# Kernel tuning notes

Measured on AMD Instinct MI355X. Metric: run time of the kernel, lower is better.

## Reference

```python
import jax, jax.numpy as jnp
import numpy as np

LATENT_DIM = 256
BOOK_SIZE = 8192


def setup_inputs() -> dict:
    key = jax.random.key(0)
    k1, k2 = jax.random.split(key)
    z_e = jax.random.normal(k1, (16, LATENT_DIM, 32, 32), dtype=jnp.float32)
    codebook = jax.random.normal(k2, (BOOK_SIZE, LATENT_DIM), dtype=jnp.float32)
    return {"z_e": z_e, "codebook": codebook}


def reference(z_e, codebook):
    # NCHW -> NHWC -> (B*H*W, D)
    flat_z = jnp.transpose(z_e, (0, 2, 3, 1)).reshape(-1, LATENT_DIM)
    # squared euclidean distance via matmul: ||z||^2 + ||e||^2 - 2 z.e
    dist = (
        jnp.sum(flat_z ** 2, axis=1, keepdims=True)
        + jnp.sum(codebook ** 2, axis=1)
        - 2.0 * flat_z @ codebook.T
    )  # (N, book_size)
    indices = jnp.argmin(dist, axis=1)          # (N,)
    z_q = codebook[indices]                      # (N, D) gather
    return z_q, indices
```

## Files before the change

### kernel.cpp

```cpp
#include <hip/hip_runtime.h>
#include <stdint.h>

#define NROWS 16384
#define NCODES 8192
#define DIM 256
#define EPS_S 0.4f
#define SM 0.8f

typedef __attribute__((ext_vector_type(8))) short bf16x8;
typedef __attribute__((ext_vector_type(4))) float f32x4;
typedef unsigned int uint32;

__device__ __forceinline__ unsigned short f2bf(float f) {
  union { float f; unsigned int u; } v; v.f = f;
  unsigned int u = v.u;
  return (unsigned short)((u + 0x7FFFu + ((u >> 16) & 1u)) >> 16);
}

__device__ __forceinline__ void glds16(const void* g, void* l) {
  __builtin_amdgcn_global_load_lds(
      (const __attribute__((address_space(1))) unsigned int*)g,
      (__attribute__((address_space(3))) unsigned int*)l, 16, 0, 0);
}

__device__ __forceinline__ unsigned long long packdi(float d, int idx) {
  unsigned int u = __float_as_uint(d);
  u = (u & 0x80000000u) ? ~u : (u | 0x80000000u);
  return ((unsigned long long)u << 32) | (unsigned int)idx;
}
__device__ __forceinline__ unsigned long long u64min(unsigned long long a,
                                                     unsigned long long b) {
  return a < b ? a : b;
}
__device__ __forceinline__ unsigned long long shflx64(unsigned long long v, int m) {
  int lo = __shfl_xor((int)(unsigned int)v, m);
  int hi = __shfl_xor((int)(v >> 32), m);
  return ((unsigned long long)(unsigned int)hi << 32) | (unsigned int)lo;
}
__device__ __forceinline__ uint32 umax(uint32 a, uint32 b) { return a > b ? a : b; }
__device__ __forceinline__ uint32 umin(uint32 a, uint32 b) { return a < b ? a : b; }

__global__ __launch_bounds__(256) void prep_z(const float* __restrict__ z,
                                              float* __restrict__ flatz,
                                              ushort* __restrict__ zb) {
  __shared__ float t[32][33];
  const int tx = threadIdx.x & 31, ty = threadIdx.x >> 5;
  const int b = blockIdx.z, ct = blockIdx.y, ht = blockIdx.x;
  const float* src = z + (size_t)b * 262144 + (size_t)(ct * 32) * 1024 + ht * 32;
#pragma unroll
  for (int i = 0; i < 4; ++i) {
    int c = ty + i * 8;
    t[c][tx] = src[c * 1024 + tx];
  }
  __syncthreads();
#pragma unroll
  for (int i = 0; i < 4; ++i) {
    int hw = ty + i * 8;
    int row = b * 1024 + ht * 32 + hw;
    float v = t[tx][hw];
    flatz[(size_t)row * 256 + ct * 32 + tx] = v;
    zb[(size_t)row * 256 + ct * 32 + tx] = f2bf(v);
  }
}

__global__ __launch_bounds__(256) void prep_cb(const float* __restrict__ cb,
                                               ushort* __restrict__ eb,
                                               float* __restrict__ enorm) {
  const int lane = threadIdx.x & 63, wave = threadIdx.x >> 6;
  const int code = blockIdx.x * 4 + wave;
  float4 v = *(const float4*)(cb + (size_t)code * 256 + lane * 4);
  ushort4 o;
  o.x = f2bf(v.x); o.y = f2bf(v.y); o.z = f2bf(v.z); o.w = f2bf(v.w);
  *(ushort4*)(eb + (size_t)code * 256 + lane * 4) = o;
  float ss = v.x * v.x + v.y * v.y + v.z * v.z + v.w * v.w;
#pragma unroll
  for (int s = 1; s < 64; s <<= 1) ss += __shfl_xor(ss, s);
  if (lane == 0) enorm[code] = ss;
}

__global__ __launch_bounds__(256) void vq_gemm(const ushort* __restrict__ eb,
                                               const ushort* __restrict__ zb,
                                               const float* __restrict__ enorm,
                                               uint32* __restrict__ bm) {
  __shared__ __align__(16) ushort As[2][4096];
  __shared__ __align__(16) ushort Bs[2][4096];
  const int tid = threadIdx.x;
  const int wave = tid >> 6, lane = tid & 63;
  const int wr = wave >> 1, wc = wave & 1;
  const int code0 = blockIdx.x * 128;
  const int zrow0 = blockIdx.y * 128;
  const int q = lane >> 4, l15 = lane & 15;
  const int slot = (q ^ ((l15 >> 1) & 3)) * 8;

  f32x4 acc[4][4];
#pragma unroll
  for (int i = 0; i < 4; ++i) {
    float4 e = *(const float4*)(enorm + code0 + wr * 64 + i * 16 + q * 4);
    f32x4 c0 = {1024.f - 0.5f * e.x, 1024.f - 0.5f * e.y,
                1024.f - 0.5f * e.z, 1024.f - 0.5f * e.w};
#pragma unroll
    for (int j = 0; j < 4; ++j) acc[i][j] = c0;
  }

  const int r_in = lane >> 2;
  const int kc = (lane & 3) ^ ((lane >> 3) & 3);
  const ushort* aG0 = eb + (size_t)(code0 + wave * 16 + r_in) * 256 + kc * 8;
  const ushort* aG1 = eb + (size_t)(code0 + 64 + wave * 16 + r_in) * 256 + kc * 8;
  const ushort* bG0 = zb + (size_t)(zrow0 + wave * 16 + r_in) * 256 + kc * 8;
  const ushort* bG1 = zb + (size_t)(zrow0 + 64 + wave * 16 + r_in) * 256 + kc * 8;

  glds16(aG0, &As[0][wave * 512]);
  glds16(aG1, &As[0][(wave + 4) * 512]);
  glds16(bG0, &Bs[0][wave * 512]);
  glds16(bG1, &Bs[0][(wave + 4) * 512]);

#pragma unroll
  for (int k0 = 0; k0 < 8; ++k0) {
    const int cur = k0 & 1;
    __syncthreads();
    if (k0 < 7) {
      glds16(aG0 + (k0 + 1) * 32, &As[cur ^ 1][wave * 512]);
      glds16(aG1 + (k0 + 1) * 32, &As[cur ^ 1][(wave + 4) * 512]);
      glds16(bG0 + (k0 + 1) * 32, &Bs[cur ^ 1][wave * 512]);
      glds16(bG1 + (k0 + 1) * 32, &Bs[cur ^ 1][(wave + 4) * 512]);
    }
    bf16x8 af[4], bf[4];
#pragma unroll
    for (int i = 0; i < 4; ++i)
      af[i] = *(const bf16x8*)(&As[cur][(wr * 64 + i * 16 + l15) * 32 + slot]);
#pragma unroll
    for (int j = 0; j < 4; ++j)
      bf[j] = *(const bf16x8*)(&Bs[cur][(wc * 64 + j * 16 + l15) * 32 + slot]);
#pragma unroll
    for (int i = 0; i < 4; ++i)
#pragma unroll
      for (int j = 0; j < 4; ++j)
        acc[i][j] = __builtin_amdgcn_mfma_f32_16x16x32_bf16(af[i], bf[j],
                                                            acc[i][j], 0, 0, 0);
  }

  const int cid0 = blockIdx.x * 8 + wr * 4;
#pragma unroll
  for (int j = 0; j < 4; ++j) {
    uint32 res[4];
#pragma unroll
    for (int i = 0; i < 4; ++i) {
      uint32 pv0 = (__float_as_uint(acc[i][j][0]) & ~31u) | (uint32)(q * 4 + 0);
      uint32 pv1 = (__float_as_uint(acc[i][j][1]) & ~31u) | (uint32)(q * 4 + 1);
      uint32 pv2 = (__float_as_uint(acc[i][j][2]) & ~31u) | (uint32)(q * 4 + 2);
      uint32 pv3 = (__float_as_uint(acc[i][j][3]) & ~31u) | (uint32)(q * 4 + 3);
      uint32 x01 = umax(pv0, pv1), n01 = umin(pv0, pv1);
      uint32 x23 = umax(pv2, pv3), n23 = umin(pv2, pv3);
      uint32 m1 = umax(x01, x23);
      uint32 m2 = umax(umin(x01, x23), umax(n01, n23));
#pragma unroll
      for (int m = 16; m < 64; m <<= 1) {
        uint32 o1 = (uint32)__shfl_xor((int)m1, m);
        uint32 o2 = (uint32)__shfl_xor((int)m2, m);
        m2 = umax(umax(m2, o2), umin(m1, o1));
        m1 = umax(m1, o1);
      }
      float s1 = __uint_as_float(m1 & ~31u);
      float s2 = __uint_as_float(m2 & ~31u);
      res[i] = (s1 - s2 > SM) ? (m1 | 16u) : m1;
    }
    if (lane < 16) {
      int zr = zrow0 + wc * 64 + j * 16 + l15;
      uint4 o; o.x = res[0]; o.y = res[1]; o.z = res[2]; o.w = res[3];
      *(uint4*)(bm + (size_t)zr * 512 + cid0) = o;
    }
  }
}

__device__ __forceinline__ unsigned long long chunk_exact(
    int chunk, const float* __restrict__ zrow, const float* __restrict__ cb,
    const float* __restrict__ enorm, int lane) {
  const int code = chunk * 16 + (lane >> 2);
  const float* zp = zrow + (lane & 3) * 64;
  const float* cp = cb + (size_t)code * 256 + (lane & 3) * 64;
  float s = 0.f;
#pragma unroll
  for (int d = 0; d < 64; d += 4) {
    float4 zv = *(const float4*)(zp + d);
    float4 cv = *(const float4*)(cp + d);
    s = fmaf(zv.x, cv.x, s); s = fmaf(zv.y, cv.y, s);
    s = fmaf(zv.z, cv.z, s); s = fmaf(zv.w, cv.w, s);
  }
  s += __shfl_xor(s, 1);
  s += __shfl_xor(s, 2);
  float dist = fmaf(-2.f, s, enorm[code]);
  unsigned long long key = ((lane & 3) == 0) ? packdi(dist, code) : ~0ull;
#pragma unroll
  for (int m = 1; m < 64; m <<= 1) key = u64min(key, shflx64(key, m));
  return key;
}

__global__ __launch_bounds__(256) void vq_sel(const uint32* __restrict__ bm,
                                              const float* __restrict__ flatz,
                                              const float* __restrict__ cb,
                                              const float* __restrict__ enorm,
                                              float* __restrict__ zq,
                                              float* __restrict__ oidx) {
  const int lane = threadIdx.x & 63;
  const int row = blockIdx.x * 4 + (threadIdx.x >> 6);
  uint4 va = *(const uint4*)(bm + (size_t)row * 512 + lane * 8);
  uint4 vb = *(const uint4*)(bm + (size_t)row * 512 + lane * 8 + 4);
  uint32 v[8] = {va.x, va.y, va.z, va.w, vb.x, vb.y, vb.z, vb.w};
  uint32 m1 = 0, m2 = 0; int ch = 0;
#pragma unroll
  for (int s = 0; s < 8; ++s) {
    uint32 pv = v[s];
    m2 = umax(m2, umin(m1, pv));
    ch = (pv > m1) ? (lane * 8 + s) : ch;
    m1 = umax(m1, pv);
  }
#pragma unroll
  for (int m = 1; m < 64; m <<= 1) {
    uint32 o1 = (uint32)__shfl_xor((int)m1, m);
    uint32 o2 = (uint32)__shfl_xor((int)m2, m);
    int oc = __shfl_xor(ch, m);
    m2 = umax(umax(m2, o2), umin(m1, o1));
    ch = (o1 > m1) ? oc : ch;
    m1 = umax(m1, o1);
  }
  float s1 = __uint_as_float(m1 & ~31u);
  float s2 = __uint_as_float(m2 & ~31u);
  int idx;
  if ((m1 & 16u) && (s1 - s2 > SM)) {
    idx = ch * 16 + (int)(m1 & 15u);
  } else {
    const float* zrow = flatz + (size_t)row * 256;
    unsigned long long key = chunk_exact(ch, zrow, cb, enorm, lane);
    float dbest;
    { unsigned int u = (unsigned int)(key >> 32);
      u = (u & 0x80000000u) ? (u & 0x7FFFFFFFu) : ~u;
      dbest = __uint_as_float(u); }
    float thr = (1024.f - 0.5f * dbest) - EPS_S;
#pragma unroll
    for (int s = 0; s < 8; ++s) {
      bool cand = __uint_as_float(v[s] & ~31u) >= thr;
      unsigned long long mk = __ballot(cand);
      while (mk) {
        int L = __ffsll(mk) - 1;
        mk &= mk - 1;
        int c2 = L * 8 + s;
        if (c2 == ch) continue;
        key = u64min(key, chunk_exact(c2, zrow, cb, enorm, lane));
      }
    }
    idx = (int)(key & 0xFFFFFFFFull);
  }
  if (lane == 0) oidx[row] = (float)idx;
  float4 val = *(const float4*)(cb + (size_t)idx * 256 + lane * 4);
  *(float4*)(zq + (size_t)row * 256 + lane * 4) = val;
}

extern "C" void kernel_launch(void* const* d_in, const int* in_sizes, int n_in,
                              void* d_out, int out_size, void* d_ws, size_t ws_size,
                              hipStream_t stream) {
  const float* z = (const float*)d_in[0];
  const float* cb = (const float*)d_in[1];
  char* ws = (char*)d_ws;
  ushort* zb = (ushort*)(ws);
  ushort* eb = (ushort*)(ws + (8u << 20));
  float* enorm = (float*)(ws + (12u << 20));
  uint32* bm = (uint32*)(ws + (13u << 20));
  float* zq = (float*)d_out;
  float* oidx = zq + (size_t)NROWS * DIM;
  float* flatz = zq;

  prep_z<<<dim3(32, 8, 16), 256, 0, stream>>>(z, flatz, zb);
  prep_cb<<<NCODES / 4, 256, 0, stream>>>(cb, eb, enorm);
  vq_gemm<<<dim3(NCODES / 128, NROWS / 128), 256, 0, stream>>>(eb, zb, enorm, bm);
  vq_sel<<<NROWS / 4, 256, 0, stream>>>(bm, flatz, cb, enorm, zq, oidx);
}
```

Measured before the change: 207.3 us.

## Switch GEMM to 32x32x16 MFMA tiles and merge prep kernels

Replaces the 16x16x32 bf16 MFMA tiling in vq_gemm with 32x32x16 MFMA instructions, using 2x2 accumulator tiles of 16 floats each. The LDS fragment loads, the swizzle and the per-16-code top-2 selection epilogue are reworked to match the new accumulator layout. The two prep kernels are also fused into one launch, which removes a kernel launch. The larger MFMA means fewer LDS reads and shuffles per FLOP, but the lane-to-code index mapping has to be exactly right for the bitmask output to stay correct.

```diff
diff --git a/kernel.cpp b/kernel.cpp
--- a/kernel.cpp
+++ b/kernel.cpp
@@ -8,7 +8,7 @@
 #define SM 0.8f
 
 typedef __attribute__((ext_vector_type(8))) short bf16x8;
-typedef __attribute__((ext_vector_type(4))) float f32x4;
+typedef __attribute__((ext_vector_type(16))) float f32x16;
 typedef unsigned int uint32;
 
 __device__ __forceinline__ unsigned short f2bf(float f) {
@@ -40,42 +40,44 @@
 __device__ __forceinline__ uint32 umax(uint32 a, uint32 b) { return a > b ? a : b; }
 __device__ __forceinline__ uint32 umin(uint32 a, uint32 b) { return a < b ? a : b; }
 
-__global__ __launch_bounds__(256) void prep_z(const float* __restrict__ z,
-                                              float* __restrict__ flatz,
-                                              ushort* __restrict__ zb) {
+__global__ __launch_bounds__(256) void prep(const float* __restrict__ z,
+                                            const float* __restrict__ cb,
+                                            float* __restrict__ flatz,
+                                            ushort* __restrict__ zb,
+                                            ushort* __restrict__ eb,
+                                            float* __restrict__ enorm) {
   __shared__ float t[32][33];
-  const int tx = threadIdx.x & 31, ty = threadIdx.x >> 5;
-  const int b = blockIdx.z, ct = blockIdx.y, ht = blockIdx.x;
-  const float* src = z + (size_t)b * 262144 + (size_t)(ct * 32) * 1024 + ht * 32;
-#pragma unroll
-  for (int i = 0; i < 4; ++i) {
-    int c = ty + i * 8;
-    t[c][tx] = src[c * 1024 + tx];
-  }
-  __syncthreads();
-#pragma unroll
-  for (int i = 0; i < 4; ++i) {
-    int hw = ty + i * 8;
-    int row = b * 1024 + ht * 32 + hw;
-    float v = t[tx][hw];
-    flatz[(size_t)row * 256 + ct * 32 + tx] = v;
-    zb[(size_t)row * 256 + ct * 32 + tx] = f2bf(v);
-  }
-}
-
-__global__ __launch_bounds__(256) void prep_cb(const float* __restrict__ cb,
-                                               ushort* __restrict__ eb,
-                                               float* __restrict__ enorm) {
-  const int lane = threadIdx.x & 63, wave = threadIdx.x >> 6;
-  const int code = blockIdx.x * 4 + wave;
-  float4 v = *(const float4*)(cb + (size_t)code * 256 + lane * 4);
-  ushort4 o;
-  o.x = f2bf(v.x); o.y = f2bf(v.y); o.z = f2bf(v.z); o.w = f2bf(v.w);
-  *(ushort4*)(eb + (size_t)code * 256 + lane * 4) = o;
-  float ss = v.x * v.x + v.y * v.y + v.z * v.z + v.w * v.w;
-#pragma unroll
-  for (int s = 1; s < 64; s <<= 1) ss += __shfl_xor(ss, s);
-  if (lane == 0) enorm[code] = ss;
+  const int blk = blockIdx.x;
+  if (blk < 4096) {
+    const int tx = threadIdx.x & 31, ty = threadIdx.x >> 5;
+    const int ht = blk & 31, ct = (blk >> 5) & 7, b = blk >> 8;
+    const float* src = z + (size_t)b * 262144 + (size_t)(ct * 32) * 1024 + ht * 32;
+#pragma unroll
+    for (int i = 0; i < 4; ++i) {
+      int c = ty + i * 8;
+      t[c][tx] = src[c * 1024 + tx];
+    }
+    __syncthreads();
+#pragma unroll
+    for (int i = 0; i < 4; ++i) {
+      int hw = ty + i * 8;
+      int row = b * 1024 + ht * 32 + hw;
+      float v = t[tx][hw];
+      flatz[(size_t)row * 256 + ct * 32 + tx] = v;
+      zb[(size_t)row * 256 + ct * 32 + tx] = f2bf(v);
+    }
+  } else {
+    const int lane = threadIdx.x & 63, wave = threadIdx.x >> 6;
+    const int code = (blk - 4096) * 4 + wave;
+    float4 v = *(const float4*)(cb + (size_t)code * 256 + lane * 4);
+    ushort4 o;
+    o.x = f2bf(v.x); o.y = f2bf(v.y); o.z = f2bf(v.z); o.w = f2bf(v.w);
+    *(ushort4*)(eb + (size_t)code * 256 + lane * 4) = o;
+    float ss = v.x * v.x + v.y * v.y + v.z * v.z + v.w * v.w;
+#pragma unroll
+    for (int s = 1; s < 64; s <<= 1) ss += __shfl_xor(ss, s);
+    if (lane == 0) enorm[code] = ss;
+  }
 }
 
 __global__ __launch_bounds__(256) void vq_gemm(const ushort* __restrict__ eb,
@@ -89,17 +91,26 @@
   const int wr = wave >> 1, wc = wave & 1;
   const int code0 = blockIdx.x * 128;
   const int zrow0 = blockIdx.y * 128;
-  const int q = lane >> 4, l15 = lane & 15;
-  const int slot = (q ^ ((l15 >> 1) & 3)) * 8;
-
-  f32x4 acc[4][4];
-#pragma unroll
-  for (int i = 0; i < 4; ++i) {
-    float4 e = *(const float4*)(enorm + code0 + wr * 64 + i * 16 + q * 4);
-    f32x4 c0 = {1024.f - 0.5f * e.x, 1024.f - 0.5f * e.y,
-                1024.f - 0.5f * e.z, 1024.f - 0.5f * e.w};
-#pragma unroll
-    for (int j = 0; j < 4; ++j) acc[i][j] = c0;
+  const int l31 = lane & 31, lg = lane >> 5;
+
+  f32x16 acc[2][2];
+#pragma unroll
+  for (int i = 0; i < 2; ++i) {
+    const float* ep = enorm + code0 + wr * 64 + i * 32 + 4 * lg;
+    float4 e0 = *(const float4*)(ep);
+    float4 e1 = *(const float4*)(ep + 8);
+    float4 e2 = *(const float4*)(ep + 16);
+    float4 e3 = *(const float4*)(ep + 24);
+    f32x16 c0;
+    c0[0]  = 1024.f - 0.5f * e0.x; c0[1]  = 1024.f - 0.5f * e0.y;
+    c0[2]  = 1024.f - 0.5f * e0.z; c0[3]  = 1024.f - 0.5f * e0.w;
+    c0[4]  = 1024.f - 0.5f * e1.x; c0[5]  = 1024.f - 0.5f * e1.y;
+    c0[6]  = 1024.f - 0.5f * e1.z; c0[7]  = 1024.f - 0.5f * e1.w;
+    c0[8]  = 1024.f - 0.5f * e2.x; c0[9]  = 1024.f - 0.5f * e2.y;
+    c0[10] = 1024.f - 0.5f * e2.z; c0[11] = 1024.f - 0.5f * e2.w;
+    c0[12] = 1024.f - 0.5f * e3.x; c0[13] = 1024.f - 0.5f * e3.y;
+    c0[14] = 1024.f - 0.5f * e3.z; c0[15] = 1024.f - 0.5f * e3.w;
+    acc[i][0] = c0; acc[i][1] = c0;
   }
 
   const int r_in = lane >> 2;
@@ -113,6 +124,10 @@
   glds16(aG1, &As[0][(wave + 4) * 512]);
   glds16(bG0, &Bs[0][wave * 512]);
   glds16(bG1, &Bs[0][(wave + 4) * 512]);
+
+  const int ra = wr * 64 + l31;
+  const int rb = wc * 64 + l31;
+  const int hash = (l31 >> 1) & 3;
 
 #pragma unroll
   for (int k0 = 0; k0 < 8; ++k0) {
@@ -124,48 +139,51 @@
       glds16(bG0 + (k0 + 1) * 32, &Bs[cur ^ 1][wave * 512]);
       glds16(bG1 + (k0 + 1) * 32, &Bs[cur ^ 1][(wave + 4) * 512]);
     }
-    bf16x8 af[4], bf[4];
-#pragma unroll
-    for (int i = 0; i < 4; ++i)
-      af[i] = *(const bf16x8*)(&As[cur][(wr * 64 + i * 16 + l15) * 32 + slot]);
-#pragma unroll
-    for (int j = 0; j < 4; ++j)
-      bf[j] = *(const bf16x8*)(&Bs[cur][(wc * 64 + j * 16 + l15) * 32 + slot]);
-#pragma unroll
-    for (int i = 0; i < 4; ++i)
-#pragma unroll
-      for (int j = 0; j < 4; ++j)
-        acc[i][j] = __builtin_amdgcn_mfma_f32_16x16x32_bf16(af[i], bf[j],
-                                                            acc[i][j], 0, 0, 0);
+    bf16x8 af[2][2], bf[2][2];
+#pragma unroll
+    for (int i = 0; i < 2; ++i)
+#pragma unroll
+      for (int h = 0; h < 2; ++h) {
+        int slot = (h * 2 + lg) ^ hash;
+        af[i][h] = *(const bf16x8*)(&As[cur][(ra + i * 32) * 32 + slot * 8]);
+        bf[i][h] = *(const bf16x8*)(&Bs[cur][(rb + i * 32) * 32 + slot * 8]);
+      }
+#pragma unroll
+    for (int h = 0; h < 2; ++h)
+#pragma unroll
+      for (int i = 0; i < 2; ++i)
+#pragma unroll
+        for (int j = 0; j < 2; ++j)
+          acc[i][j] = __builtin_amdgcn_mfma_f32_32x32x16_bf16(
+              af[i][h], bf[j][h], acc[i][j], 0, 0, 0);
   }
 
   const int cid0 = blockIdx.x * 8 + wr * 4;
 #pragma unroll
-  for (int j = 0; j < 4; ++j) {
+  for (int j = 0; j < 2; ++j) {
     uint32 res[4];
 #pragma unroll
-    for (int i = 0; i < 4; ++i) {
-      uint32 pv0 = (__float_as_uint(acc[i][j][0]) & ~31u) | (uint32)(q * 4 + 0);
-      uint32 pv1 = (__float_as_uint(acc[i][j][1]) & ~31u) | (uint32)(q * 4 + 1);
-      uint32 pv2 = (__float_as_uint(acc[i][j][2]) & ~31u) | (uint32)(q * 4 + 2);
-      uint32 pv3 = (__float_as_uint(acc[i][j][3]) & ~31u) | (uint32)(q * 4 + 3);
-      uint32 x01 = umax(pv0, pv1), n01 = umin(pv0, pv1);
-      uint32 x23 = umax(pv2, pv3), n23 = umin(pv2, pv3);
-      uint32 m1 = umax(x01, x23);
-      uint32 m2 = umax(umin(x01, x23), umax(n01, n23));
-#pragma unroll
-      for (int m = 16; m < 64; m <<= 1) {
-        uint32 o1 = (uint32)__shfl_xor((int)m1, m);
-        uint32 o2 = (uint32)__shfl_xor((int)m2, m);
+    for (int i = 0; i < 2; ++i)
+#pragma unroll
+      for (int hc = 0; hc < 2; ++hc) {
+        uint32 m1 = 0, m2 = 0;
+#pragma unroll
+        for (int p = 0; p < 8; ++p) {
+          uint32 id = (uint32)((p & 3) | (lg << 2) | ((p >> 2) << 3));
+          uint32 pv = (__float_as_uint(acc[i][j][hc * 8 + p]) & ~31u) | id;
+          m2 = umax(m2, umin(m1, pv));
+          m1 = umax(m1, pv);
+        }
+        uint32 o1 = (uint32)__shfl_xor((int)m1, 32);
+        uint32 o2 = (uint32)__shfl_xor((int)m2, 32);
         m2 = umax(umax(m2, o2), umin(m1, o1));
         m1 = umax(m1, o1);
+        float s1 = __uint_as_float(m1 & ~31u);
+        float s2 = __uint_as_float(m2 & ~31u);
+        res[i * 2 + hc] = (s1 - s2 > SM) ? (m1 | 16u) : m1;
       }
-      float s1 = __uint_as_float(m1 & ~31u);
-      float s2 = __uint_as_float(m2 & ~31u);
-      res[i] = (s1 - s2 > SM) ? (m1 | 16u) : m1;
-    }
-    if (lane < 16) {
-      int zr = zrow0 + wc * 64 + j * 16 + l15;
+    if (lane < 32) {
+      int zr = zrow0 + wc * 64 + j * 32 + l31;
       uint4 o; o.x = res[0]; o.y = res[1]; o.z = res[2]; o.w = res[3];
       *(uint4*)(bm + (size_t)zr * 512 + cid0) = o;
     }
@@ -269,8 +287,7 @@
   float* oidx = zq + (size_t)NROWS * DIM;
   float* flatz = zq;
 
-  prep_z<<<dim3(32, 8, 16), 256, 0, stream>>>(z, flatz, zb);
-  prep_cb<<<NCODES / 4, 256, 0, stream>>>(cb, eb, enorm);
+  prep<<<4096 + NCODES / 4, 256, 0, stream>>>(z, cb, flatz, zb, eb, enorm);
   vq_gemm<<<dim3(NCODES / 128, NROWS / 128), 256, 0, stream>>>(eb, zb, enorm, bm);
   vq_sel<<<NROWS / 4, 256, 0, stream>>>(bm, flatz, cb, enorm, zq, oidx);
 }
```

Result: faster. 198.6 us (-4.2%).
